# Performance work log

Hardware: AMD Instinct MI355X
Metric: run time of the kernel (lower is better)

Reference implementation:

```python
import jax, jax.numpy as jnp
import numpy as np

EPS = 1e-5      # BatchNorm eps
SLOPE = 0.2     # LeakyReLU negative slope
K = 20          # hardcoded k in Net
OUT_CH = 64     # AGConv out_channels
IN_CH = 6       # AGConv in_channels (= 2*3)


def _bn(x, gamma, beta, axis):
    # Inference-mode BatchNorm: running_mean=0, running_var=1
    shape = [1] * x.ndim
    shape[axis] = -1
    scale = (gamma / jnp.sqrt(1.0 + EPS)).reshape(shape)
    return x * scale + beta.reshape(shape)


def _lrelu(x):
    return jnp.where(x >= 0, x, SLOPE * x)


def _graph_feature(x, k):
    # x: (B, C, N) -> feature (B, 2C, N, k) as in get_graph_feature
    B, C, N = x.shape
    xt = jnp.swapaxes(x, 1, 2)                        # (B, N, C)
    inner = -2.0 * jnp.einsum('bci,bcj->bij', x, x)   # (B, N, N)
    xx = jnp.sum(x * x, axis=1)                       # (B, N)
    pd = -xx[:, :, None] - inner - xx[:, None, :]     # -||xi-xj||^2
    idx = jax.lax.top_k(pd, k)[1]                     # (B, N, k) nearest neighbors
    b_idx = jnp.arange(B)[:, None, None]
    nbr = xt[b_idx, idx]                              # (B, N, k, C) gather
    center = jnp.broadcast_to(xt[:, :, None, :], nbr.shape)
    feat = jnp.concatenate([nbr - center, center], axis=-1)  # (B, N, k, 2C)
    return jnp.moveaxis(feat, -1, 1)                  # (B, 2C, N, k)


def setup_inputs() -> dict:
    key = jax.random.key(0)
    ks = jax.random.split(key, 5)
    B, N = 4, 4096
    x = jax.random.normal(ks[0], (B, 3, N), dtype=jnp.float32)
    w0 = jax.random.normal(ks[1], (OUT_CH, IN_CH), dtype=jnp.float32) * 0.2
    w1 = jax.random.normal(ks[2], (OUT_CH * IN_CH, OUT_CH), dtype=jnp.float32) * 0.05
    w_out = jax.random.normal(ks[3], (3, OUT_CH), dtype=jnp.float32) * 0.1
    return {
        'x': x,
        'w0': w0, 'g0': jnp.ones(OUT_CH), 'b0': jnp.zeros(OUT_CH),
        'w1': w1, 'g1': jnp.ones(OUT_CH), 'b1': jnp.zeros(OUT_CH),
        'w_out': w_out, 'g_out': jnp.ones(3), 'b_out': jnp.zeros(3),
    }


def reference(x, w0, g0, b0, w1, g1, b1, w_out, g_out, b_out):
    # x: (B, 3, N). feat == both `x` and `p` in the torch code (points is x,
    # same idx), so compute once.
    feat = _graph_feature(x, K)                       # (B, 6, N, k)
    B, _, N, k = feat.shape
    # AGConv: weight-generating branch
    y = jnp.einsum('oc,bcnk->bonk', w0, feat)         # conv0 1x1
    y = _lrelu(_bn(y, g0, b0, 1))
    y = jnp.einsum('oc,bcnk->bonk', w1, y)            # conv1 1x1 -> (B, 384, N, k)
    y = jnp.moveaxis(y, 1, -1).reshape(B, N, k, OUT_CH, IN_CH)
    xg = jnp.moveaxis(feat, 1, -1)                    # (B, N, k, 6)
    z = jnp.einsum('bnkoc,bnkc->bnko', y, xg)         # per-edge dynamic matmul
    z = jnp.moveaxis(z, -1, 1)                        # (B, 64, N, k)
    z = _lrelu(_bn(z, g1, b1, 1))
    x1 = jnp.max(z, axis=-1)                          # max over neighbors -> (B, 64, N)
    out = jnp.einsum('oc,bcn->bon', w_out, x1)        # Net.conv1 1x1
    out = _lrelu(_bn(out, g_out, b_out, 1))
    return out
```

## Files before the change

### kernel.cpp

```cpp
#include <hip/hip_runtime.h>
#include <hip/hip_bf16.h>

#define NPTS 4096
#define BATCH 4
#define KNN 20

typedef __attribute__((ext_vector_type(8))) short bf16x8;
typedef __attribute__((ext_vector_type(4))) float f32x4;
typedef __attribute__((ext_vector_type(4))) int i32x4;
typedef unsigned long long u64;

#define OFF_W0S   0
#define OFF_B0F   384
#define OFF_S1F   448
#define OFF_B1F   512
#define OFF_WOUTS 576
#define OFF_BOUTF 768
#define OFF_WHI_BYTES 4096
#define OFF_WLO_BYTES 53248
#define OFF_IDX_BYTES 102400
#define OFF_XQ_BYTES  757760

__device__ __forceinline__ u64 shflx64(u64 v, int off) {
  int lo = __shfl_xor((int)(v & 0xFFFFFFFFull), off);
  int hi = __shfl_xor((int)(v >> 32), off);
  return ((u64)(unsigned)hi << 32) | (unsigned)lo;
}
__device__ __forceinline__ u64 shflbc64(u64 v, int src) {
  int lo = __shfl((int)(v & 0xFFFFFFFFull), src);
  int hi = __shfl((int)(v >> 32), src);
  return ((u64)(unsigned)hi << 32) | (unsigned)lo;
}

__global__ __launch_bounds__(256) void prep_kernel(
    const float* __restrict__ x,
    const float* __restrict__ w0, const float* __restrict__ g0, const float* __restrict__ b0,
    const float* __restrict__ w1, const float* __restrict__ g1, const float* __restrict__ b1,
    const float* __restrict__ wout, const float* __restrict__ gout, const float* __restrict__ bout,
    float* __restrict__ wsf, unsigned short* __restrict__ whi, unsigned short* __restrict__ wlo,
    float4* __restrict__ xq) {
  const float rs = 1.0f / sqrtf(1.0f + 1e-5f);
  int t = blockIdx.x * 256 + threadIdx.x;
  if (t < 384) wsf[OFF_W0S + t] = w0[t] * (g0[t / 6] * rs);
  if (t < 64) {
    wsf[OFF_B0F + t] = b0[t];
    wsf[OFF_S1F + t] = g1[t] * rs;
    wsf[OFF_B1F + t] = b1[t];
  }
  if (t < 192) wsf[OFF_WOUTS + t] = wout[t] * (gout[t / 64] * rs);
  if (t < 3) wsf[OFF_BOUTF + t] = bout[t];
  if (t < BATCH * NPTS) {
    int bb = t >> 12, j = t & (NPTS - 1);
    const float* xb = x + bb * 3 * NPTS;
    float x0 = xb[j], x1 = xb[NPTS + j], x2 = xb[2 * NPTS + j];
    float xx = x0 * x0 + x1 * x1 + x2 * x2;
    xq[t] = make_float4(x0, x1, x2, xx);
  }
  if (t < 24576) {
    int j = t & 7, L = (t >> 3) & 63, ft = t >> 9;
    int kk = ft >> 2, nt = ft & 3;
    int k = kk * 32 + ((L >> 4) << 3) + j;
    int c = k >> 6, d = k & 63;
    int o = nt * 16 + (L & 15);
    float w = w1[(o * 6 + c) * 64 + d];
    unsigned bw = __float_as_uint(w);
    unsigned hb = bw & 0xFFFF0000u;
    float r = w - __uint_as_float(hb);
    whi[t] = (unsigned short)(bw >> 16);
    wlo[t] = (unsigned short)(__float_as_uint(r) >> 16);
  }
}

__global__ __launch_bounds__(256) void knn_kernel(const float4* __restrict__ xq,
                                                  unsigned short* __restrict__ idxbuf) {
  __shared__ float4 tile[1024];
  const int tid = threadIdx.x;
  const int wv = tid >> 6;
  const int lane = tid & 63;
  const int pt = blockIdx.x * 4 + wv;
  const int b = pt >> 12, n = pt & (NPTS - 1);
  const float4* xqb = xq + b * NPTS;
  const float4 xin = xqb[n];
  const float xi0 = xin.x, xi1 = xin.y, xi2 = xin.z;
  const float nxxi = -xin.w;

  u64 k1 = 0, k2 = 0;
  unsigned lo = 4095u - (unsigned)lane;
#pragma unroll 1
  for (int t = 0; t < 4; ++t) {
    __syncthreads();
#pragma unroll
    for (int u = 0; u < 4; ++u) tile[u * 256 + tid] = xqb[t * 1024 + u * 256 + tid];
    __syncthreads();
#pragma unroll 4
    for (int i = 0; i < 16; ++i) {
      float4 q = tile[i * 64 + lane];
      float dot = xi0 * q.x + xi1 * q.y + xi2 * q.z;
      float pd = fmaf(2.0f, dot, nxxi) - q.w;
      u64 k = ((u64)(~__float_as_uint(pd)) << 32) | lo;
      lo -= 64u;
      bool c1 = k > k1;
      bool c2 = k > k2;
      u64 tt = c1 ? k1 : k;
      k2 = c2 ? tt : k2;
      k1 = c1 ? k : k1;
    }
  }

  u64 tk = 0;
  unsigned myout = 0;
#pragma unroll 1
  for (int r = 0; r < KNN; ++r) {
    u64 bk = k1;
    for (int off = 32; off > 0; off >>= 1) {
      u64 ok = shflx64(bk, off);
      if (ok > bk) bk = ok;
    }
    unsigned bj = 4095u - (unsigned)(bk & 4095u);
    if (lane == r) myout = bj;
    bool owner = (k1 == bk);
    u64 bit = 1ull << (bj >> 6);
    if (owner) {
      tk |= bit;
      k1 = k2;
      k2 = 0;
    }
    bool need = owner && (k1 == 0);
    u64 nm = __ballot(need);
    if (nm) {
      int LN = __ffsll(nm) - 1;
      int j2 = lane * 64 + LN;
      float4 q = xqb[j2];
      float dot = xi0 * q.x + xi1 * q.y + xi2 * q.z;
      float pd = fmaf(2.0f, dot, nxxi) - q.w;
      u64 kk = ((u64)(~__float_as_uint(pd)) << 32) | (4095u - (unsigned)j2);
      u64 tkl = shflbc64(tk, LN);
      if ((tkl >> lane) & 1) kk = 0;
      u64 w1k = kk;
      for (int off = 32; off > 0; off >>= 1) {
        u64 ok = shflx64(w1k, off);
        if (ok > w1k) w1k = ok;
      }
      u64 kk2 = (kk == w1k) ? 0 : kk;
      u64 w2k = kk2;
      for (int off = 32; off > 0; off >>= 1) {
        u64 ok = shflx64(w2k, off);
        if (ok > w2k) w2k = ok;
      }
      if (lane == LN) { k1 = w1k; k2 = w2k; }
    }
  }
  if (lane < KNN) idxbuf[pt * KNN + lane] = (unsigned short)myout;
}

__global__ __launch_bounds__(64, 2) void mlp_kernel(const float4* __restrict__ xq,
                                                    const float* __restrict__ wsf,
                                                    const unsigned short* __restrict__ whi,
                                                    const unsigned short* __restrict__ wlo,
                                                    const unsigned short* __restrict__ idxbuf,
                                                    float* __restrict__ out) {
  __shared__ float w0l[448];
  __shared__ float v6l[80 * 12];
  __shared__ float pmax[20 * 66];

  const int lane = threadIdx.x;
  const int quad = lane >> 4, l15 = lane & 15;
  const int pt_base = blockIdx.x * 4;

  const i32x4* whp = (const i32x4*)whi;
  const i32x4* wlp = (const i32x4*)wlo;

  i32x4 wh[4], wl[4];
#pragma unroll
  for (int nt = 0; nt < 4; ++nt) {
    wh[nt] = whp[nt * 64 + lane];
    wl[nt] = wlp[nt * 64 + lane];
  }

  for (int i = lane; i < 448; i += 64) w0l[i] = wsf[i];

#pragma unroll
  for (int rep = 0; rep < 2; ++rep) {
    int e = rep * 64 + lane;
    if (e < 80) {
      int p = e / 20, el = e - p * 20;
      int pt = pt_base + p;
      int b = pt >> 12, n = pt & (NPTS - 1);
      float4 xi = xq[b * NPTS + n];
      int jn = idxbuf[pt * KNN + el];
      float4 xj = xq[b * NPTS + jn];
      v6l[e * 12 + 0] = xj.x - xi.x;
      v6l[e * 12 + 1] = xj.y - xi.y;
      v6l[e * 12 + 2] = xj.z - xi.z;
      v6l[e * 12 + 3] = xi.x;
      v6l[e * 12 + 4] = xi.y;
      v6l[e * 12 + 5] = xi.z;
    }
  }
  __syncthreads();

  f32x4 acc[5][4];
#pragma unroll
  for (int t = 0; t < 5; ++t)
#pragma unroll
    for (int nt = 0; nt < 4; ++nt) acc[t][nt] = (f32x4){0.f, 0.f, 0.f, 0.f};

#pragma unroll 1
  for (int hh = 0; hh < 2; ++hh) {
    float v6r[5][6];
#pragma unroll
    for (int t = 0; t < 5; ++t) {
      const float* vr = v6l + (t * 16 + l15) * 12;
      f32x4 a4 = *(const f32x4*)vr;
      v6r[t][0] = a4.x; v6r[t][1] = a4.y; v6r[t][2] = a4.z; v6r[t][3] = a4.w;
      v6r[t][4] = vr[4]; v6r[t][5] = vr[5];
    }
    float hf[5][8];
#pragma unroll
    for (int j = 0; j < 8; ++j) {
      const int d = hh * 32 + quad * 8 + j;
      const float* wr = w0l + d * 6;
      float wc0 = wr[0], wc1 = wr[1], wc2 = wr[2];
      float wc3 = wr[3], wc4 = wr[4], wc5 = wr[5];
      float bb = w0l[384 + d];
#pragma unroll
      for (int t = 0; t < 5; ++t) {
        float a = bb + wc0 * v6r[t][0] + wc1 * v6r[t][1] + wc2 * v6r[t][2]
                     + wc3 * v6r[t][3] + wc4 * v6r[t][4] + wc5 * v6r[t][5];
        hf[t][j] = fmaxf(a, 0.2f * a);
      }
    }

#pragma unroll 1
    for (int cc = 0; cc < 6; ++cc) {
      const int kk = cc * 2 + hh;
      const bool hasnext = !(hh == 1 && cc == 5);
      const int kkn = (cc < 5) ? kk + 2 : 1;
      i32x4 whn[4], wln[4];
      if (hasnext) {
#pragma unroll
        for (int nt = 0; nt < 4; ++nt) {
          whn[nt] = whp[(kkn * 4 + nt) * 64 + lane];
          wln[nt] = wlp[(kkn * 4 + nt) * 64 + lane];
        }
      }
#pragma unroll
      for (int t = 0; t < 5; ++t) {
        float vc = v6l[(t * 16 + l15) * 12 + cc];
        float u0 = vc * hf[t][0], u1 = vc * hf[t][1];
        float u2 = vc * hf[t][2], u3 = vc * hf[t][3];
        float u4 = vc * hf[t][4], u5 = vc * hf[t][5];
        float u6 = vc * hf[t][6], u7 = vc * hf[t][7];
        unsigned ub0 = __float_as_uint(u0), ub1 = __float_as_uint(u1);
        unsigned ub2 = __float_as_uint(u2), ub3 = __float_as_uint(u3);
        unsigned ub4 = __float_as_uint(u4), ub5 = __float_as_uint(u5);
        unsigned ub6 = __float_as_uint(u6), ub7 = __float_as_uint(u7);
        float r0 = u0 - __uint_as_float(ub0 & 0xFFFF0000u);
        float r1 = u1 - __uint_as_float(ub1 & 0xFFFF0000u);
        float r2 = u2 - __uint_as_float(ub2 & 0xFFFF0000u);
        float r3 = u3 - __uint_as_float(ub3 & 0xFFFF0000u);
        float r4 = u4 - __uint_as_float(ub4 & 0xFFFF0000u);
        float r5 = u5 - __uint_as_float(ub5 & 0xFFFF0000u);
        float r6 = u6 - __uint_as_float(ub6 & 0xFFFF0000u);
        float r7 = u7 - __uint_as_float(ub7 & 0xFFFF0000u);
        i32x4 ah, al;
        ah.x = __builtin_amdgcn_perm(ub1, ub0, 0x07060302);
        ah.y = __builtin_amdgcn_perm(ub3, ub2, 0x07060302);
        ah.z = __builtin_amdgcn_perm(ub5, ub4, 0x07060302);
        ah.w = __builtin_amdgcn_perm(ub7, ub6, 0x07060302);
        al.x = __builtin_amdgcn_perm(__float_as_uint(r1), __float_as_uint(r0), 0x07060302);
        al.y = __builtin_amdgcn_perm(__float_as_uint(r3), __float_as_uint(r2), 0x07060302);
        al.z = __builtin_amdgcn_perm(__float_as_uint(r5), __float_as_uint(r4), 0x07060302);
        al.w = __builtin_amdgcn_perm(__float_as_uint(r7), __float_as_uint(r6), 0x07060302);
        bf16x8 ahv = __builtin_bit_cast(bf16x8, ah);
        bf16x8 alv = __builtin_bit_cast(bf16x8, al);
#pragma unroll
        for (int nt = 0; nt < 4; ++nt) {
          bf16x8 bh = __builtin_bit_cast(bf16x8, wh[nt]);
          bf16x8 bl = __builtin_bit_cast(bf16x8, wl[nt]);
          acc[t][nt] = __builtin_amdgcn_mfma_f32_16x16x32_bf16(ahv, bh, acc[t][nt], 0, 0, 0);
          acc[t][nt] = __builtin_amdgcn_mfma_f32_16x16x32_bf16(ahv, bl, acc[t][nt], 0, 0, 0);
          acc[t][nt] = __builtin_amdgcn_mfma_f32_16x16x32_bf16(alv, bh, acc[t][nt], 0, 0, 0);
        }
      }
      if (hasnext) {
#pragma unroll
        for (int nt = 0; nt < 4; ++nt) { wh[nt] = whn[nt]; wl[nt] = wln[nt]; }
      }
    }
  }
  __syncthreads();

  float s1v[4], b1v[4];
#pragma unroll
  for (int nt = 0; nt < 4; ++nt) {
    s1v[nt] = wsf[OFF_S1F + nt * 16 + l15];
    b1v[nt] = wsf[OFF_B1F + nt * 16 + l15];
  }
#pragma unroll
  for (int t = 0; t < 5; ++t) {
#pragma unroll
    for (int nt = 0; nt < 4; ++nt) {
      f32x4 a = acc[t][nt];
      float z0 = a.x * s1v[nt] + b1v[nt]; z0 = fmaxf(z0, 0.2f * z0);
      float z1 = a.y * s1v[nt] + b1v[nt]; z1 = fmaxf(z1, 0.2f * z1);
      float z2 = a.z * s1v[nt] + b1v[nt]; z2 = fmaxf(z2, 0.2f * z2);
      float z3 = a.w * s1v[nt] + b1v[nt]; z3 = fmaxf(z3, 0.2f * z3);
      float m4 = fmaxf(fmaxf(z0, z1), fmaxf(z2, z3));
      pmax[(t * 4 + quad) * 66 + nt * 16 + l15] = m4;
    }
  }
  __syncthreads();

  float woutr[3];
#pragma unroll
  for (int m = 0; m < 3; ++m) woutr[m] = wsf[OFF_WOUTS + m * 64 + lane];
#pragma unroll
  for (int p = 0; p < 4; ++p) {
    float x1 = pmax[(p * 5 + 0) * 66 + lane];
    x1 = fmaxf(x1, pmax[(p * 5 + 1) * 66 + lane]);
    x1 = fmaxf(x1, pmax[(p * 5 + 2) * 66 + lane]);
    x1 = fmaxf(x1, pmax[(p * 5 + 3) * 66 + lane]);
    x1 = fmaxf(x1, pmax[(p * 5 + 4) * 66 + lane]);
    int pt = pt_base + p;
    int b = pt >> 12, n = pt & (NPTS - 1);
#pragma unroll
    for (int m = 0; m < 3; ++m) {
      float part = woutr[m] * x1;
      for (int off = 32; off > 0; off >>= 1) part += __shfl_xor(part, off);
      if (lane == 0) {
        float ov = part + wsf[OFF_BOUTF + m];
        out[(b * 3 + m) * NPTS + n] = fmaxf(ov, 0.2f * ov);
      }
    }
  }
}

extern "C" void kernel_launch(void* const* d_in, const int* in_sizes, int n_in,
                              void* d_out, int out_size, void* d_ws, size_t ws_size,
                              hipStream_t stream) {
  const float* x    = (const float*)d_in[0];
  const float* w0   = (const float*)d_in[1];
  const float* g0   = (const float*)d_in[2];
  const float* b0   = (const float*)d_in[3];
  const float* w1   = (const float*)d_in[4];
  const float* g1   = (const float*)d_in[5];
  const float* b1   = (const float*)d_in[6];
  const float* wout = (const float*)d_in[7];
  const float* gout = (const float*)d_in[8];
  const float* bout = (const float*)d_in[9];
  float* wsf = (float*)d_ws;
  unsigned short* whi = (unsigned short*)((char*)d_ws + OFF_WHI_BYTES);
  unsigned short* wlo = (unsigned short*)((char*)d_ws + OFF_WLO_BYTES);
  unsigned short* idxbuf = (unsigned short*)((char*)d_ws + OFF_IDX_BYTES);
  float4* xq = (float4*)((char*)d_ws + OFF_XQ_BYTES);
  float* out = (float*)d_out;

  prep_kernel<<<96, 256, 0, stream>>>(x, w0, g0, b0, w1, g1, b1, wout, gout, bout,
                                      wsf, whi, wlo, xq);
  knn_kernel<<<BATCH * NPTS / 4, 256, 0, stream>>>(xq, idxbuf);
  mlp_kernel<<<BATCH * NPTS / 4, 64, 0, stream>>>(xq, wsf, whi, wlo, idxbuf, out);
}
```

Before: 193.0 us.

## Fuse kNN and MLP kernels into one block, splitting MLP tiles across waves

Merges the kNN and MLP kernels into one kernel of 256 threads. Each block computes the kNN indices of 4 points and keeps them in shared memory, so the index buffer round trip through global memory and one kernel launch go away. The MLP work is split across the 4 waves: wave 0 handles two 16-edge tiles and the others one each, and each wave then writes the output for its own point. The kNN scan now reads the point array directly from global/L2 instead of staging it in an LDS tile, and the MLP tiles are imbalanced across waves, which may leave three waves idle while wave 0 finishes.

```diff
diff --git a/kernel.cpp b/kernel.cpp
--- a/kernel.cpp
+++ b/kernel.cpp
@@ -18,7 +18,6 @@
 #define OFF_BOUTF 768
 #define OFF_WHI_BYTES 4096
 #define OFF_WLO_BYTES 53248
-#define OFF_IDX_BYTES 102400
 #define OFF_XQ_BYTES  757760
 
 __device__ __forceinline__ u64 shflx64(u64 v, int off) {
@@ -71,40 +70,45 @@
   }
 }
 
-__global__ __launch_bounds__(256) void knn_kernel(const float4* __restrict__ xq,
-                                                  unsigned short* __restrict__ idxbuf) {
-  __shared__ float4 tile[1024];
+__global__ __launch_bounds__(256) void fused_kernel(const float4* __restrict__ xq,
+                                                    const float* __restrict__ wsf,
+                                                    const unsigned short* __restrict__ whi,
+                                                    const unsigned short* __restrict__ wlo,
+                                                    float* __restrict__ out) {
+  __shared__ float w0l[448];
+  __shared__ float v6l[80 * 12];
+  __shared__ float pmax[20 * 66];
+  __shared__ unsigned short idxl[80];
+
   const int tid = threadIdx.x;
   const int wv = tid >> 6;
   const int lane = tid & 63;
-  const int pt = blockIdx.x * 4 + wv;
+  const int quad = lane >> 4, l15 = lane & 15;
+  const int pt_base = blockIdx.x * 4;
+  const int pt = pt_base + wv;
   const int b = pt >> 12, n = pt & (NPTS - 1);
   const float4* xqb = xq + b * NPTS;
+
+  for (int i = tid; i < 448; i += 256) w0l[i] = wsf[i];
+
   const float4 xin = xqb[n];
   const float xi0 = xin.x, xi1 = xin.y, xi2 = xin.z;
   const float nxxi = -xin.w;
 
   u64 k1 = 0, k2 = 0;
   unsigned lo = 4095u - (unsigned)lane;
-#pragma unroll 1
-  for (int t = 0; t < 4; ++t) {
-    __syncthreads();
-#pragma unroll
-    for (int u = 0; u < 4; ++u) tile[u * 256 + tid] = xqb[t * 1024 + u * 256 + tid];
-    __syncthreads();
 #pragma unroll 4
-    for (int i = 0; i < 16; ++i) {
-      float4 q = tile[i * 64 + lane];
-      float dot = xi0 * q.x + xi1 * q.y + xi2 * q.z;
-      float pd = fmaf(2.0f, dot, nxxi) - q.w;
-      u64 k = ((u64)(~__float_as_uint(pd)) << 32) | lo;
-      lo -= 64u;
-      bool c1 = k > k1;
-      bool c2 = k > k2;
-      u64 tt = c1 ? k1 : k;
-      k2 = c2 ? tt : k2;
-      k1 = c1 ? k : k1;
-    }
+  for (int s = 0; s < 64; ++s) {
+    float4 q = xqb[s * 64 + lane];
+    float dot = xi0 * q.x + xi1 * q.y + xi2 * q.z;
+    float pd = fmaf(2.0f, dot, nxxi) - q.w;
+    u64 k = ((u64)(~__float_as_uint(pd)) << 32) | lo;
+    lo -= 64u;
+    bool c1 = k > k1;
+    bool c2 = k > k2;
+    u64 tt = c1 ? k1 : k;
+    k2 = c2 ? tt : k2;
+    k1 = c1 ? k : k1;
   }
 
   u64 tk = 0;
@@ -150,26 +154,10 @@
       if (lane == LN) { k1 = w1k; k2 = w2k; }
     }
   }
-  if (lane < KNN) idxbuf[pt * KNN + lane] = (unsigned short)myout;
-}
-
-__global__ __launch_bounds__(64, 2) void mlp_kernel(const float4* __restrict__ xq,
-                                                    const float* __restrict__ wsf,
-                                                    const unsigned short* __restrict__ whi,
-                                                    const unsigned short* __restrict__ wlo,
-                                                    const unsigned short* __restrict__ idxbuf,
-                                                    float* __restrict__ out) {
-  __shared__ float w0l[448];
-  __shared__ float v6l[80 * 12];
-  __shared__ float pmax[20 * 66];
-
-  const int lane = threadIdx.x;
-  const int quad = lane >> 4, l15 = lane & 15;
-  const int pt_base = blockIdx.x * 4;
+  if (lane < KNN) idxl[wv * KNN + lane] = (unsigned short)myout;
 
   const i32x4* whp = (const i32x4*)whi;
   const i32x4* wlp = (const i32x4*)wlo;
-
   i32x4 wh[4], wl[4];
 #pragma unroll
   for (int nt = 0; nt < 4; ++nt) {
@@ -177,80 +165,80 @@
     wl[nt] = wlp[nt * 64 + lane];
   }
 
-  for (int i = lane; i < 448; i += 64) w0l[i] = wsf[i];
-
-#pragma unroll
-  for (int rep = 0; rep < 2; ++rep) {
-    int e = rep * 64 + lane;
-    if (e < 80) {
-      int p = e / 20, el = e - p * 20;
-      int pt = pt_base + p;
-      int b = pt >> 12, n = pt & (NPTS - 1);
-      float4 xi = xq[b * NPTS + n];
-      int jn = idxbuf[pt * KNN + el];
-      float4 xj = xq[b * NPTS + jn];
-      v6l[e * 12 + 0] = xj.x - xi.x;
-      v6l[e * 12 + 1] = xj.y - xi.y;
-      v6l[e * 12 + 2] = xj.z - xi.z;
-      v6l[e * 12 + 3] = xi.x;
-      v6l[e * 12 + 4] = xi.y;
-      v6l[e * 12 + 5] = xi.z;
-    }
-  }
   __syncthreads();
 
-  f32x4 acc[5][4];
-#pragma unroll
-  for (int t = 0; t < 5; ++t)
-#pragma unroll
-    for (int nt = 0; nt < 4; ++nt) acc[t][nt] = (f32x4){0.f, 0.f, 0.f, 0.f};
-
+  if (tid < 80) {
+    int p = tid / 20;
+    int ptg = pt_base + p;
+    int bb = ptg >> 12, nn = ptg & (NPTS - 1);
+    float4 xi = xq[bb * NPTS + nn];
+    int jn = idxl[tid];
+    float4 xj = xq[bb * NPTS + jn];
+    v6l[tid * 12 + 0] = xj.x - xi.x;
+    v6l[tid * 12 + 1] = xj.y - xi.y;
+    v6l[tid * 12 + 2] = xj.z - xi.z;
+    v6l[tid * 12 + 3] = xi.x;
+    v6l[tid * 12 + 4] = xi.y;
+    v6l[tid * 12 + 5] = xi.z;
+  }
+  __syncthreads();
+
+  float s1v[4], b1v[4];
+#pragma unroll
+  for (int nt = 0; nt < 4; ++nt) {
+    s1v[nt] = wsf[OFF_S1F + nt * 16 + l15];
+    b1v[nt] = wsf[OFF_B1F + nt * 16 + l15];
+  }
+
+  const int ntile = (wv == 0) ? 2 : 1;
 #pragma unroll 1
-  for (int hh = 0; hh < 2; ++hh) {
-    float v6r[5][6];
-#pragma unroll
-    for (int t = 0; t < 5; ++t) {
-      const float* vr = v6l + (t * 16 + l15) * 12;
-      f32x4 a4 = *(const f32x4*)vr;
-      v6r[t][0] = a4.x; v6r[t][1] = a4.y; v6r[t][2] = a4.z; v6r[t][3] = a4.w;
-      v6r[t][4] = vr[4]; v6r[t][5] = vr[5];
-    }
-    float hf[5][8];
-#pragma unroll
-    for (int j = 0; j < 8; ++j) {
-      const int d = hh * 32 + quad * 8 + j;
-      const float* wr = w0l + d * 6;
-      float wc0 = wr[0], wc1 = wr[1], wc2 = wr[2];
-      float wc3 = wr[3], wc4 = wr[4], wc5 = wr[5];
-      float bb = w0l[384 + d];
-#pragma unroll
-      for (int t = 0; t < 5; ++t) {
-        float a = bb + wc0 * v6r[t][0] + wc1 * v6r[t][1] + wc2 * v6r[t][2]
-                     + wc3 * v6r[t][3] + wc4 * v6r[t][4] + wc5 * v6r[t][5];
-        hf[t][j] = fmaxf(a, 0.2f * a);
-      }
-    }
+  for (int rep = 0; rep < ntile; ++rep) {
+    const int t = (rep == 0) ? wv : 4;
+    const int row = t * 16 + l15;
+    const float* vr = v6l + row * 12;
+    float v60 = vr[0], v61 = vr[1], v62 = vr[2];
+    float v63 = vr[3], v64 = vr[4], v65 = vr[5];
+
+    if (rep == 1) {
+#pragma unroll
+      for (int nt = 0; nt < 4; ++nt) {
+        wh[nt] = whp[nt * 64 + lane];
+        wl[nt] = wlp[nt * 64 + lane];
+      }
+    }
+
+    f32x4 acc[4];
+#pragma unroll
+    for (int nt = 0; nt < 4; ++nt) acc[nt] = (f32x4){0.f, 0.f, 0.f, 0.f};
 
 #pragma unroll 1
-    for (int cc = 0; cc < 6; ++cc) {
-      const int kk = cc * 2 + hh;
-      const bool hasnext = !(hh == 1 && cc == 5);
-      const int kkn = (cc < 5) ? kk + 2 : 1;
-      i32x4 whn[4], wln[4];
-      if (hasnext) {
-#pragma unroll
-        for (int nt = 0; nt < 4; ++nt) {
-          whn[nt] = whp[(kkn * 4 + nt) * 64 + lane];
-          wln[nt] = wlp[(kkn * 4 + nt) * 64 + lane];
+    for (int hh = 0; hh < 2; ++hh) {
+      float hf[8];
+#pragma unroll
+      for (int j = 0; j < 8; ++j) {
+        const int d = hh * 32 + quad * 8 + j;
+        const float* wr = w0l + d * 6;
+        float a = w0l[384 + d] + wr[0] * v60 + wr[1] * v61 + wr[2] * v62
+                               + wr[3] * v63 + wr[4] * v64 + wr[5] * v65;
+        hf[j] = fmaxf(a, 0.2f * a);
+      }
+
+#pragma unroll 1
+      for (int cc = 0; cc < 6; ++cc) {
+        const int kk = cc * 2 + hh;
+        const bool hasnext = !(hh == 1 && cc == 5);
+        const int kkn = (cc < 5) ? kk + 2 : 1;
+        i32x4 whn[4], wln[4];
+        if (hasnext) {
+#pragma unroll
+          for (int nt = 0; nt < 4; ++nt) {
+            whn[nt] = whp[(kkn * 4 + nt) * 64 + lane];
+            wln[nt] = wlp[(kkn * 4 + nt) * 64 + lane];
+          }
         }
-      }
-#pragma unroll
-      for (int t = 0; t < 5; ++t) {
-        float vc = v6l[(t * 16 + l15) * 12 + cc];
-        float u0 = vc * hf[t][0], u1 = vc * hf[t][1];
-        float u2 = vc * hf[t][2], u3 = vc * hf[t][3];
-        float u4 = vc * hf[t][4], u5 = vc * hf[t][5];
-        float u6 = vc * hf[t][6], u7 = vc * hf[t][7];
+        float vc = v6l[row * 12 + cc];
+        float u0 = vc * hf[0], u1 = vc * hf[1], u2 = vc * hf[2], u3 = vc * hf[3];
+        float u4 = vc * hf[4], u5 = vc * hf[5], u6 = vc * hf[6], u7 = vc * hf[7];
         unsigned ub0 = __float_as_uint(u0), ub1 = __float_as_uint(u1);
         unsigned ub2 = __float_as_uint(u2), ub3 = __float_as_uint(u3);
         unsigned ub4 = __float_as_uint(u4), ub5 = __float_as_uint(u5);
@@ -278,30 +266,20 @@
         for (int nt = 0; nt < 4; ++nt) {
           bf16x8 bh = __builtin_bit_cast(bf16x8, wh[nt]);
           bf16x8 bl = __builtin_bit_cast(bf16x8, wl[nt]);
-          acc[t][nt] = __builtin_amdgcn_mfma_f32_16x16x32_bf16(ahv, bh, acc[t][nt], 0, 0, 0);
-          acc[t][nt] = __builtin_amdgcn_mfma_f32_16x16x32_bf16(ahv, bl, acc[t][nt], 0, 0, 0);
-          acc[t][nt] = __builtin_amdgcn_mfma_f32_16x16x32_bf16(alv, bh, acc[t][nt], 0, 0, 0);
+          acc[nt] = __builtin_amdgcn_mfma_f32_16x16x32_bf16(ahv, bh, acc[nt], 0, 0, 0);
+          acc[nt] = __builtin_amdgcn_mfma_f32_16x16x32_bf16(ahv, bl, acc[nt], 0, 0, 0);
+          acc[nt] = __builtin_amdgcn_mfma_f32_16x16x32_bf16(alv, bh, acc[nt], 0, 0, 0);
         }
-      }
-      if (hasnext) {
-#pragma unroll
-        for (int nt = 0; nt < 4; ++nt) { wh[nt] = whn[nt]; wl[nt] = wln[nt]; }
-      }
-    }
-  }
-  __syncthreads();
-
-  float s1v[4], b1v[4];
-#pragma unroll
-  for (int nt = 0; nt < 4; ++nt) {
-    s1v[nt] = wsf[OFF_S1F + nt * 16 + l15];
-    b1v[nt] = wsf[OFF_B1F + nt * 16 + l15];
-  }
-#pragma unroll
-  for (int t = 0; t < 5; ++t) {
+        if (hasnext) {
+#pragma unroll
+          for (int nt = 0; nt < 4; ++nt) { wh[nt] = whn[nt]; wl[nt] = wln[nt]; }
+        }
+      }
+    }
+
 #pragma unroll
     for (int nt = 0; nt < 4; ++nt) {
-      f32x4 a = acc[t][nt];
+      f32x4 a = acc[nt];
       float z0 = a.x * s1v[nt] + b1v[nt]; z0 = fmaxf(z0, 0.2f * z0);
       float z1 = a.y * s1v[nt] + b1v[nt]; z1 = fmaxf(z1, 0.2f * z1);
       float z2 = a.z * s1v[nt] + b1v[nt]; z2 = fmaxf(z2, 0.2f * z2);
@@ -312,21 +290,15 @@
   }
   __syncthreads();
 
-  float woutr[3];
-#pragma unroll
-  for (int m = 0; m < 3; ++m) woutr[m] = wsf[OFF_WOUTS + m * 64 + lane];
-#pragma unroll
-  for (int p = 0; p < 4; ++p) {
-    float x1 = pmax[(p * 5 + 0) * 66 + lane];
-    x1 = fmaxf(x1, pmax[(p * 5 + 1) * 66 + lane]);
-    x1 = fmaxf(x1, pmax[(p * 5 + 2) * 66 + lane]);
-    x1 = fmaxf(x1, pmax[(p * 5 + 3) * 66 + lane]);
-    x1 = fmaxf(x1, pmax[(p * 5 + 4) * 66 + lane]);
-    int pt = pt_base + p;
-    int b = pt >> 12, n = pt & (NPTS - 1);
+  {
+    float x1 = pmax[(wv * 5 + 0) * 66 + lane];
+    x1 = fmaxf(x1, pmax[(wv * 5 + 1) * 66 + lane]);
+    x1 = fmaxf(x1, pmax[(wv * 5 + 2) * 66 + lane]);
+    x1 = fmaxf(x1, pmax[(wv * 5 + 3) * 66 + lane]);
+    x1 = fmaxf(x1, pmax[(wv * 5 + 4) * 66 + lane]);
 #pragma unroll
     for (int m = 0; m < 3; ++m) {
-      float part = woutr[m] * x1;
+      float part = wsf[OFF_WOUTS + m * 64 + lane] * x1;
       for (int off = 32; off > 0; off >>= 1) part += __shfl_xor(part, off);
       if (lane == 0) {
         float ov = part + wsf[OFF_BOUTF + m];
@@ -352,12 +324,10 @@
   float* wsf = (float*)d_ws;
   unsigned short* whi = (unsigned short*)((char*)d_ws + OFF_WHI_BYTES);
   unsigned short* wlo = (unsigned short*)((char*)d_ws + OFF_WLO_BYTES);
-  unsigned short* idxbuf = (unsigned short*)((char*)d_ws + OFF_IDX_BYTES);
   float4* xq = (float4*)((char*)d_ws + OFF_XQ_BYTES);
   float* out = (float*)d_out;
 
   prep_kernel<<<96, 256, 0, stream>>>(x, w0, g0, b0, w1, g1, b1, wout, gout, bout,
                                       wsf, whi, wlo, xq);
-  knn_kernel<<<BATCH * NPTS / 4, 256, 0, stream>>>(xq, idxbuf);
-  mlp_kernel<<<BATCH * NPTS / 4, 64, 0, stream>>>(xq, wsf, whi, wlo, idxbuf, out);
-}
+  fused_kernel<<<BATCH * NPTS / 4, 256, 0, stream>>>(xq, wsf, whi, wlo, out);
+}
```

Result: slower. 237.2 us (+22.9%).
